# Kernel optimization log

Hardware: AMD Instinct MI355X
Metric: run time of the kernel (lower is better)

The kernel has to match this reference:

```python
import jax, jax.numpy as jnp
import numpy as np

H_IMG = 128; W_IMG = 128
TANFOVX = 0.5; TANFOVY = 0.5
SCALE_MOD = 1.0
C0 = 0.28209479177387814
C1 = 0.4886025119029199
C2 = (1.0925484305920792, -1.0925484305920792, 0.31539156525252005, -1.0925484305920792, 0.5462742152960396)
C3 = (-0.5900435899266435, 2.890611442640554, -0.4570457994644658, 0.3731763325901154, -0.4570457994644658, 1.445305721320277, -0.5900435899266435)


def quat_to_rot(q):
    q = q / jnp.linalg.norm(q, axis=-1, keepdims=True)
    r, x, y, z = q[..., 0], q[..., 1], q[..., 2], q[..., 3]
    row0 = jnp.stack([1 - 2 * (y * y + z * z), 2 * (x * y - r * z), 2 * (x * z + r * y)], -1)
    row1 = jnp.stack([2 * (x * y + r * z), 1 - 2 * (x * x + z * z), 2 * (y * z - r * x)], -1)
    row2 = jnp.stack([2 * (x * z - r * y), 2 * (y * z + r * x), 1 - 2 * (x * x + y * y)], -1)
    return jnp.stack([row0, row1, row2], -2)  # [P,3,3]


def eval_sh(sh, d):
    # sh: [P,16,3], d: [P,3] unit view directions -> RGB per gaussian (degree 3)
    x, y, z = d[:, 0:1], d[:, 1:2], d[:, 2:3]
    res = C0 * sh[:, 0]
    res = res - C1 * y * sh[:, 1] + C1 * z * sh[:, 2] - C1 * x * sh[:, 3]
    xx, yy, zz = x * x, y * y, z * z
    xy, yz, xz = x * y, y * z, x * z
    res = (res + C2[0] * xy * sh[:, 4] + C2[1] * yz * sh[:, 5]
           + C2[2] * (2 * zz - xx - yy) * sh[:, 6] + C2[3] * xz * sh[:, 7]
           + C2[4] * (xx - yy) * sh[:, 8])
    res = (res + C3[0] * y * (3 * xx - yy) * sh[:, 9] + C3[1] * xy * z * sh[:, 10]
           + C3[2] * y * (4 * zz - xx - yy) * sh[:, 11]
           + C3[3] * z * (2 * zz - 3 * xx - 3 * yy) * sh[:, 12]
           + C3[4] * x * (4 * zz - xx - yy) * sh[:, 13]
           + C3[5] * z * (xx - yy) * sh[:, 14] + C3[6] * x * (xx - 3 * yy) * sh[:, 15])
    return jnp.maximum(res + 0.5, 0.0)


def _render_one(means, sh, opac, scales, rots, bg, target, view, proj, campos):
    P = means.shape[0]
    fx = W_IMG / (2.0 * TANFOVX)
    fy = H_IMG / (2.0 * TANFOVY)
    ones = jnp.ones((P, 1), means.dtype)
    xyz1 = jnp.concatenate([means, ones], axis=1)
    hom = xyz1 @ proj.T                                   # [P,4]
    p_w = 1.0 / (hom[:, 3] + 1e-7)
    p_proj = hom[:, :3] * p_w[:, None]
    p_view = xyz1 @ view.T
    depth = p_view[:, 2]
    in_front = depth > 0.2

    # 3D covariance: Sigma = R diag(s) (R diag(s))^T
    R = quat_to_rot(rots)
    M = R * (scales * SCALE_MOD)[:, None, :]
    Sigma = M @ jnp.swapaxes(M, 1, 2)                     # [P,3,3]

    # EWA Jacobian -> 2D covariance
    tz = depth
    txc = jnp.clip(p_view[:, 0] / tz, -1.3 * TANFOVX, 1.3 * TANFOVX) * tz
    tyc = jnp.clip(p_view[:, 1] / tz, -1.3 * TANFOVY, 1.3 * TANFOVY) * tz
    zp = jnp.zeros_like(tz)
    J = jnp.stack([jnp.stack([fx / tz, zp, -fx * txc / (tz * tz)], -1),
                   jnp.stack([zp, fy / tz, -fy * tyc / (tz * tz)], -1)], -2)  # [P,2,3]
    T = J @ view[:3, :3]
    cov2d = T @ Sigma @ jnp.swapaxes(T, 1, 2)             # [P,2,2]
    c00 = cov2d[:, 0, 0] + 0.3
    c11 = cov2d[:, 1, 1] + 0.3
    c01 = cov2d[:, 0, 1]
    det = c00 * c11 - c01 * c01
    valid = in_front & (det > 1e-12)
    inv_det = 1.0 / jnp.where(det > 1e-12, det, 1.0)
    conic = jnp.stack([c11 * inv_det, -c01 * inv_det, c00 * inv_det], -1)
    mid = 0.5 * (c00 + c11)
    lam = mid + jnp.sqrt(jnp.maximum(mid * mid - det, 0.1))
    radii = jnp.where(valid, jnp.ceil(3.0 * jnp.sqrt(lam)), 0.0)

    # NDC -> pixel centers
    px = ((p_proj[:, 0] + 1.0) * W_IMG - 1.0) * 0.5
    py = ((p_proj[:, 1] + 1.0) * H_IMG - 1.0) * 0.5

    dirs = means - campos[None]
    dirs = dirs / jnp.linalg.norm(dirs, axis=-1, keepdims=True)
    colors = eval_sh(sh, dirs)                            # [P,3]

    # front-to-back depth order (same per-pixel order as the tile sort)
    order = jnp.argsort(depth)
    inv_order = jnp.argsort(order)
    px_s, py_s = px[order], py[order]
    con_s = conic[order]
    col_s = colors[order]
    op_s = opac[order, 0]
    val_s = valid[order]

    xs = jnp.arange(W_IMG, dtype=means.dtype)
    ys = jnp.arange(H_IMG, dtype=means.dtype)
    dx = px_s[:, None, None] - xs[None, None, :]          # [P,1,W] -> [P,H,W]
    dy = py_s[:, None, None] - ys[None, :, None]
    power = (-0.5 * (con_s[:, 0, None, None] * dx * dx + con_s[:, 2, None, None] * dy * dy)
             - con_s[:, 1, None, None] * dx * dy)         # [P,H,W]
    alpha = jnp.minimum(0.99, op_s[:, None, None] * jnp.exp(jnp.minimum(power, 0.0)))
    keep = (power <= 0.0) & (alpha >= 1.0 / 255.0) & val_s[:, None, None]
    alpha = jnp.where(keep, alpha, 0.0)
    trans = jnp.cumprod(1.0 - alpha, axis=0)
    T_exc = jnp.concatenate([jnp.ones((1, H_IMG, W_IMG), alpha.dtype), trans[:-1]], axis=0)
    w = alpha * T_exc                                     # per-gaussian pixel weights
    T_final = trans[-1]
    color = jnp.einsum('phw,pc->chw', w, col_s) + T_final[None] * bg[:, None, None]
    alpha_img = (1.0 - T_final)[None]
    est_color = jnp.einsum('phw,chw->pc', w, target)[inv_order]
    est_weight = w.sum(axis=(1, 2))[inv_order, None]
    return color, alpha_img, est_color, est_weight, radii


def reference(means3D, sh, opacities, scales, rotations, target_image, bg, viewmatrix, projmatrix, campos):
    f = jax.vmap(_render_one, in_axes=(0, 0, 0, 0, 0, 0, 0, None, None, None))
    return f(means3D, sh, opacities, scales, rotations, bg, target_image, viewmatrix, projmatrix, campos)


def setup_inputs() -> dict:
    key = jax.random.key(0)
    ks = jax.random.split(key, 8)
    B, P, K = 2, 1024, 16
    xy = jax.random.normal(ks[0], (B, P, 2), jnp.float32) * 1.5
    z = jax.random.uniform(ks[1], (B, P, 1), jnp.float32, 2.0, 6.0)
    means3D = jnp.concatenate([xy, z], -1)
    sh = jax.random.normal(ks[2], (B, P, K, 3), jnp.float32) * 0.3
    opacities = jax.random.uniform(ks[3], (B, P, 1), jnp.float32)
    scales = jax.random.uniform(ks[4], (B, P, 3), jnp.float32, 0.01, 0.08)
    rotations = jax.random.normal(ks[5], (B, P, 4), jnp.float32)
    target_image = jax.random.uniform(ks[6], (B, 3, H_IMG, W_IMG), jnp.float32)
    bg = jax.random.uniform(ks[7], (B, 3), jnp.float32)
    view = np.eye(4, dtype=np.float32)  # camera at origin, +z forward
    znear, zfar = 0.01, 100.0
    proj = np.zeros((4, 4), np.float32)
    proj[0, 0] = 1.0 / TANFOVX
    proj[1, 1] = 1.0 / TANFOVY
    proj[2, 2] = zfar / (zfar - znear)
    proj[2, 3] = -(zfar * znear) / (zfar - znear)
    proj[3, 2] = 1.0
    return {"means3D": means3D, "sh": sh, "opacities": opacities, "scales": scales,
            "rotations": rotations, "target_image": target_image, "bg": bg,
            "viewmatrix": jnp.asarray(view), "projmatrix": jnp.asarray(proj @ view),
            "campos": jnp.zeros((3,), jnp.float32)}
```

## Files before the change

### kernel.cpp

```cpp
#include <hip/hip_runtime.h>
#include <math.h>

#define HI 128
#define WI 128
#define BB 2
#define PG 1024
#define NE (BB*PG)
#define NTILES 128
#define NRED 16
#define MAGIC_HI 0xFEEDFACECAFE0000ULL
#define MASK_HI  0xFFFFFFFFFFFF0000ULL

#define OFF_ALPHA (BB*3*HI*WI)
#define OFF_ESTC  (OFF_ALPHA + BB*HI*WI)
#define OFF_ESTW  (OFF_ESTC + BB*PG*3)
#define OFF_RADII (OFF_ESTW + BB*PG)

struct PC {
  float px, py, ex, ey;
  float A, B, C, op;
  unsigned key;
  float radii;
};

__device__ __forceinline__ PC proj_cull(int e,
    const float* __restrict__ means, const float* __restrict__ opac,
    const float* __restrict__ scales, const float* __restrict__ rots,
    const float* __restrict__ vm, const float* __restrict__ pm)
{
  PC o;
  float mx = means[e*3+0], my = means[e*3+1], mz = means[e*3+2];

  float hom0 = pm[0]*mx + pm[1]*my + pm[2]*mz + pm[3];
  float hom1 = pm[4]*mx + pm[5]*my + pm[6]*mz + pm[7];
  float hom3 = pm[12]*mx + pm[13]*my + pm[14]*mz + pm[15];
  float p_w  = 1.0f / (hom3 + 1e-7f);
  float pp0 = hom0 * p_w, pp1 = hom1 * p_w;

  float pv0   = vm[0]*mx + vm[1]*my + vm[2]*mz  + vm[3];
  float pv1   = vm[4]*mx + vm[5]*my + vm[6]*mz  + vm[7];
  float depth = vm[8]*mx + vm[9]*my + vm[10]*mz + vm[11];

  float qr = rots[e*4+0], qx = rots[e*4+1], qy = rots[e*4+2], qz = rots[e*4+3];
  float qn = sqrtf(qr*qr + qx*qx + qy*qy + qz*qz);
  qr /= qn; qx /= qn; qy /= qn; qz /= qn;
  float R00 = 1.0f-2.0f*(qy*qy+qz*qz), R01 = 2.0f*(qx*qy-qr*qz), R02 = 2.0f*(qx*qz+qr*qy);
  float R10 = 2.0f*(qx*qy+qr*qz), R11 = 1.0f-2.0f*(qx*qx+qz*qz), R12 = 2.0f*(qy*qz-qr*qx);
  float R20 = 2.0f*(qx*qz-qr*qy), R21 = 2.0f*(qy*qz+qr*qx), R22 = 1.0f-2.0f*(qx*qx+qy*qy);

  float s0 = scales[e*3+0], s1 = scales[e*3+1], s2 = scales[e*3+2];
  float M00=R00*s0, M01=R01*s1, M02=R02*s2;
  float M10=R10*s0, M11=R11*s1, M12=R12*s2;
  float M20=R20*s0, M21=R21*s1, M22=R22*s2;
  float S00 = M00*M00+M01*M01+M02*M02;
  float S01 = M00*M10+M01*M11+M02*M12;
  float S02 = M00*M20+M01*M21+M02*M22;
  float S11 = M10*M10+M11*M11+M12*M12;
  float S12 = M10*M20+M11*M21+M12*M22;
  float S22 = M20*M20+M21*M21+M22*M22;

  const float fx = 128.0f, fyc = 128.0f;
  float tz = depth;
  float txc = fminf(fmaxf(pv0/tz, -0.65f), 0.65f) * tz;
  float tyc = fminf(fmaxf(pv1/tz, -0.65f), 0.65f) * tz;
  float J00 = fx/tz,  J02 = -fx*txc/(tz*tz);
  float J11 = fyc/tz, J12 = -fyc*tyc/(tz*tz);

  float T00 = J00*vm[0] + J02*vm[8];
  float T01 = J00*vm[1] + J02*vm[9];
  float T02 = J00*vm[2] + J02*vm[10];
  float T10 = J11*vm[4] + J12*vm[8];
  float T11 = J11*vm[5] + J12*vm[9];
  float T12 = J11*vm[6] + J12*vm[10];

  float TS00 = T00*S00 + T01*S01 + T02*S02;
  float TS01 = T00*S01 + T01*S11 + T02*S12;
  float TS02 = T00*S02 + T01*S12 + T02*S22;
  float TS10 = T10*S00 + T11*S01 + T12*S02;
  float TS11 = T10*S01 + T11*S11 + T12*S12;
  float TS12 = T10*S02 + T11*S12 + T12*S22;

  float c00 = TS00*T00 + TS01*T01 + TS02*T02 + 0.3f;
  float c01 = TS00*T10 + TS01*T11 + TS02*T12;
  float c11 = TS10*T10 + TS11*T11 + TS12*T12 + 0.3f;

  float det = c00*c11 - c01*c01;
  bool valid = (depth > 0.2f) && (det > 1e-12f);
  float inv_det = 1.0f / (det > 1e-12f ? det : 1.0f);
  o.A =  c11 * inv_det;
  o.B = -c01 * inv_det;
  o.C =  c00 * inv_det;
  float mid = 0.5f * (c00 + c11);
  float lam = mid + sqrtf(fmaxf(mid*mid - det, 0.1f));
  o.radii = valid ? ceilf(3.0f * sqrtf(lam)) : 0.0f;

  o.px = ((pp0 + 1.0f)*WI - 1.0f)*0.5f;
  o.py = ((pp1 + 1.0f)*HI - 1.0f)*0.5f;

  float opv = opac[e];
  o.op = opv;
  float tau = logf(255.0f * opv);
  bool rok = valid && (tau > 0.0f);
  o.ex = rok ? sqrtf(2.0f*tau*c00) + 0.02f : -1e9f;
  o.ey = rok ? sqrtf(2.0f*tau*c11) + 0.02f : -1e9f;

  unsigned u = __float_as_uint(depth);
  o.key = (u >> 31) ? ~u : (u | 0x80000000u);
  return o;
}

__device__ __forceinline__ void sh_color(int e,
    const float* __restrict__ sh, const float* __restrict__ means,
    const float* __restrict__ campos, float col[3])
{
  float mx = means[e*3+0], my = means[e*3+1], mz = means[e*3+2];
  float dxr = mx - campos[0], dyr = my - campos[1], dzr = mz - campos[2];
  float dn = sqrtf(dxr*dxr + dyr*dyr + dzr*dzr);
  float x = dxr/dn, y = dyr/dn, z = dzr/dn;
  float xx=x*x, yy=y*y, zz=z*z, xy=x*y, yz=y*z, xz=x*z;
  const float* S = sh + e*48;
  #pragma unroll
  for (int c = 0; c < 3; ++c) {
    float r = 0.28209479177387814f * S[0+c];
    r -= 0.4886025119029199f * y * S[3+c];
    r += 0.4886025119029199f * z * S[6+c];
    r -= 0.4886025119029199f * x * S[9+c];
    r += 1.0925484305920792f  * xy * S[12+c];
    r += -1.0925484305920792f * yz * S[15+c];
    r += 0.31539156525252005f * (2.0f*zz-xx-yy) * S[18+c];
    r += -1.0925484305920792f * xz * S[21+c];
    r += 0.5462742152960396f  * (xx-yy) * S[24+c];
    r += -0.5900435899266435f * y * (3.0f*xx-yy) * S[27+c];
    r += 2.890611442640554f   * xy * z * S[30+c];
    r += -0.4570457994644658f * y * (4.0f*zz-xx-yy) * S[33+c];
    r += 0.3731763325901154f  * z * (2.0f*zz-3.0f*xx-3.0f*yy) * S[36+c];
    r += -0.4570457994644658f * x * (4.0f*zz-xx-yy) * S[39+c];
    r += 1.445305721320277f   * z * (xx-yy) * S[42+c];
    r += -0.5900435899266435f * x * (xx-3.0f*yy) * S[45+c];
    col[c] = fmaxf(r + 0.5f, 0.0f);
  }
}

__global__ __launch_bounds__(256) void fused_kernel(
    const float* __restrict__ means, const float* __restrict__ sh,
    const float* __restrict__ opac, const float* __restrict__ scales,
    const float* __restrict__ rots, const float* __restrict__ vm,
    const float* __restrict__ pm, const float* __restrict__ campos,
    const float* __restrict__ target, const float* __restrict__ bg,
    float4* __restrict__ pval, unsigned long long* __restrict__ flags,
    int* __restrict__ pgid, float* __restrict__ out)
{
  const int t = threadIdx.x;
  const int blk = blockIdx.x;

  __shared__ unsigned long long skey[PG];
  __shared__ float4 recA[256], recB[256], colC[256], stgt[256];
  __shared__ float  wmat[32][264];
  __shared__ int    scount;
  __shared__ int    scnt[64], soff[65];

  if (blk < NTILES) {
    const int b = blk >> 6, tile = blk & 63;
    const int tx0i = (tile & 7) * 16, ty0i = (tile >> 3) * 16;
    const int xi = tx0i + (t & 15), yi = ty0i + (t >> 4);
    const float fxp = (float)xi, fyp = (float)yi;
    const float rx0 = (float)tx0i, ry0 = (float)ty0i;

    if (t == 0) scount = 0;
    stgt[t] = make_float4(target[((b*3+0)*HI + yi)*WI + xi],
                          target[((b*3+1)*HI + yi)*WI + xi],
                          target[((b*3+2)*HI + yi)*WI + xi], 1.0f);
    __syncthreads();

    for (int k = 0; k < 4; ++k) {
      int ci = k*256 + t;
      PC r = proj_cull((b<<10)+ci, means, opac, scales, rots, vm, pm);
      bool ok = (r.px + r.ex >= rx0) && (r.px - r.ex <= rx0 + 15.0f)
             && (r.py + r.ey >= ry0) && (r.py - r.ey <= ry0 + 15.0f);
      if (ok) {
        int pos = atomicAdd(&scount, 1);
        skey[pos] = (((unsigned long long)r.key) << 10) | (unsigned)ci;
      }
    }
    __syncthreads();
    int total = scount;

    if (total > 1) {
      if (total <= 64) {
        if (t < 64) {
          unsigned long long v = (t < total) ? skey[t] : ~0ull;
          #pragma unroll
          for (int k = 2; k <= 64; k <<= 1) {
            bool dirAsc = ((t & k) == 0);
            #pragma unroll
            for (int j = k >> 1; j > 0; j >>= 1) {
              unsigned long long o = __shfl_xor(v, j, 64);
              bool takeMin = (((t & j) == 0) == dirAsc);
              bool less = v < o;
              v = (takeMin == less) ? v : o;
            }
          }
          if (t < total) skey[t] = v;
        }
        __syncthreads();
      } else {
        int M = 64; while (M < total) M <<= 1;
        for (int i = total + t; i < M; i += 256) skey[i] = ~0ull;
        __syncthreads();
        for (int k = 2; k <= M; k <<= 1)
          for (int j = k >> 1; j > 0; j >>= 1) {
            for (int base = t; base < M; base += 256) {
              int ixj = base ^ j;
              if (ixj > base) {
                unsigned long long a = skey[base], q = skey[ixj];
                bool up = ((base & k) == 0);
                if ((a > q) == up) { skey[base] = q; skey[ixj] = a; }
              }
            }
            __syncthreads();
          }
      }
    }

    float T = 1.0f, a0 = 0.f, a1 = 0.f, a2 = 0.f;

    for (int p0 = 0; p0 < total; p0 += 256) {
      int lim = min(256, total - p0);
      if (p0 + t < total) {
        int gi = (int)(skey[p0 + t] & 1023u);
        int e = (b<<10) + gi;
        PC r = proj_cull(e, means, opac, scales, rots, vm, pm);
        float col[3]; sh_color(e, sh, means, campos, col);
        recA[t] = make_float4(r.px, r.py, r.A, r.B);
        recB[t] = make_float4(r.C, r.op, __int_as_float(gi), 0.f);
        colC[t] = make_float4(col[0], col[1], col[2], 0.f);
      }
      __syncthreads();

      for (int c0 = 0; c0 < lim; c0 += 32) {
        int cc = min(32, lim - c0);
        for (int i = 0; i < cc; ++i) {
          float4 qa = recA[c0+i], qb = recB[c0+i], qc = colC[c0+i];
          float dx = qa.x - fxp, dy = qa.y - fyp;
          float power = -0.5f*(qa.z*dx*dx + qb.x*dy*dy) - qa.w*dx*dy;
          float alpha = fminf(0.99f, qb.y * __expf(power));
          bool keep = (power <= 0.0f) && (alpha >= (1.0f/255.0f));
          float w_ = keep ? alpha * T : 0.0f;
          a0 += w_*qc.x; a1 += w_*qc.y; a2 += w_*qc.z;
          T -= w_;
          wmat[i][t] = w_;
        }
        __syncthreads();
        int row = t >> 3, j = t & 7;
        if (row < cc) {
          float e0=0.f, e1=0.f, e2=0.f, ew=0.f;
          #pragma unroll 8
          for (int k = 0; k < 32; ++k) {
            int p = j + 8*k;
            float w_ = wmat[row][p];
            float4 tg = stgt[p];
            e0 += w_*tg.x; e1 += w_*tg.y; e2 += w_*tg.z; ew += w_;
          }
          #pragma unroll
          for (int o = 4; o; o >>= 1) {
            e0 += __shfl_down(e0, o, 8); e1 += __shfl_down(e1, o, 8);
            e2 += __shfl_down(e2, o, 8); ew += __shfl_down(ew, o, 8);
          }
          if (j == 0) {
            int idx = p0 + c0 + row;
            pgid[blk*PG + idx] = __float_as_int(recB[c0+row].z);
            pval[blk*PG + idx] = make_float4(e0, e1, e2, ew);
          }
        }
        __syncthreads();
      }
    }

    out[((b*3+0)*HI + yi)*WI + xi] = a0 + T * bg[b*3+0];
    out[((b*3+1)*HI + yi)*WI + xi] = a1 + T * bg[b*3+1];
    out[((b*3+2)*HI + yi)*WI + xi] = a2 + T * bg[b*3+2];
    out[OFF_ALPHA + (b*HI + yi)*WI + xi] = 1.0f - T;

    __syncthreads();
    if (t == 0) {
      __threadfence();
      atomicExch(&flags[blk], MAGIC_HI | (unsigned long long)total);
    }
    return;
  }

  const int r = blk - NTILES;
  const int batch = r >> 3, seg = r & 7;

  if (t < 128) {
    int e_own = (batch<<10) + seg*128 + t;
    PC g = proj_cull(e_own, means, opac, scales, rots, vm, pm);
    out[OFF_RADII + e_own] = g.radii;
  }

  float* acc = &wmat[0][0];
  for (int i = t; i < 128*4; i += 256) acc[i] = 0.f;

  if (t < 64) {
    unsigned long long v;
    do { v = atomicAdd(&flags[batch*64 + t], 0ull); }
    while ((v & MASK_HI) != MAGIC_HI);
    scnt[t] = (int)(v & 0xFFFFull);
  }
  __syncthreads();
  __threadfence();

  if (t == 0) {
    int s = 0;
    for (int i = 0; i < 64; ++i) { soff[i] = s; s += scnt[i]; }
    soff[64] = s;
  }
  __syncthreads();
  int E = soff[64];

  for (int idx = t; idx < E; idx += 256) {
    int lo = 0, hi = 63;
    while (lo < hi) { int mid = (lo+hi+1) >> 1; if (soff[mid] <= idx) lo = mid; else hi = mid-1; }
    int tb = batch*64 + lo;
    int j = idx - soff[lo];
    int gi = pgid[tb*PG + j];
    if ((gi >> 7) == seg) {
      float4 v = pval[tb*PG + j];
      int s = gi & 127;
      atomicAdd(&acc[s*4+0], v.x);
      atomicAdd(&acc[s*4+1], v.y);
      atomicAdd(&acc[s*4+2], v.z);
      atomicAdd(&acc[s*4+3], v.w);
    }
  }
  __syncthreads();

  if (t < 128) {
    int e_own = (batch<<10) + seg*128 + t;
    out[OFF_ESTC + e_own*3 + 0] = acc[t*4+0];
    out[OFF_ESTC + e_own*3 + 1] = acc[t*4+1];
    out[OFF_ESTC + e_own*3 + 2] = acc[t*4+2];
    out[OFF_ESTW + e_own]       = acc[t*4+3];
  }
}

extern "C" void kernel_launch(void* const* d_in, const int* in_sizes, int n_in,
                              void* d_out, int out_size, void* d_ws, size_t ws_size,
                              hipStream_t stream) {
  const float* means  = (const float*)d_in[0];
  const float* sh     = (const float*)d_in[1];
  const float* opac   = (const float*)d_in[2];
  const float* scales = (const float*)d_in[3];
  const float* rots   = (const float*)d_in[4];
  const float* target = (const float*)d_in[5];
  const float* bg     = (const float*)d_in[6];
  const float* vm     = (const float*)d_in[7];
  const float* pm     = (const float*)d_in[8];
  const float* campos = (const float*)d_in[9];
  float* out = (float*)d_out;

  float4* pval = (float4*)d_ws;
  unsigned long long* flags = (unsigned long long*)(pval + NTILES*PG);
  int* pgid = (int*)(flags + NTILES);

  fused_kernel<<<NTILES + NRED, 256, 0, stream>>>(
      means, sh, opac, scales, rots, vm, pm, campos, target, bg,
      pval, flags, pgid, out);
}
```

Baseline: 21.57 us.

## Compute per-Gaussian projection and SH once in producer blocks, share via workspace

Sixteen producer blocks now project, cull and evaluate SH colour for each Gaussian once, writing the results to global workspace, then signal with flags. Tile blocks wait on those flags, then read the precomputed records instead of recomputing proj_cull for all 1024 Gaussians plus SH per tile. The producer blocks later also do the per-Gaussian reduction, spinning with s_sleep on tile flags. This removes heavy redundant per-tile math but adds a cross-block dependency and spin-wait latency, and it relies on producer blocks being scheduled first. Flags are never reset, so the scheme is only safe if the workspace is cleared between launches.

Result: slower. 27.86 us (+29.2%).

```diff
diff --git a/kernel.cpp b/kernel.cpp
--- a/kernel.cpp
+++ b/kernel.cpp
@@ -6,10 +6,11 @@
 #define BB 2
 #define PG 1024
 #define NE (BB*PG)
+#define NPROD 16
 #define NTILES 128
-#define NRED 16
-#define MAGIC_HI 0xFEEDFACECAFE0000ULL
-#define MASK_HI  0xFFFFFFFFFFFF0000ULL
+#define MAGIC     0xFEEDFACECAFEBEEFULL
+#define MAGIC_HI  0xFEEDFACECAFE0000ULL
+#define MASK_HI   0xFFFFFFFFFFFF0000ULL
 
 #define OFF_ALPHA (BB*3*HI*WI)
 #define OFF_ESTC  (OFF_ALPHA + BB*HI*WI)
@@ -147,8 +148,13 @@
     const float* __restrict__ rots, const float* __restrict__ vm,
     const float* __restrict__ pm, const float* __restrict__ campos,
     const float* __restrict__ target, const float* __restrict__ bg,
-    float4* __restrict__ pval, unsigned long long* __restrict__ flags,
-    int* __restrict__ pgid, float* __restrict__ out)
+    float4* __restrict__ culk, unsigned int* __restrict__ keyar,
+    float4* __restrict__ recAg, float4* __restrict__ recBg,
+    float4* __restrict__ colCg,
+    float4* __restrict__ pval, int* __restrict__ pgid,
+    unsigned long long* __restrict__ prodflags,
+    unsigned long long* __restrict__ tileflags,
+    float* __restrict__ out)
 {
   const int t = threadIdx.x;
   const int blk = blockIdx.x;
@@ -159,188 +165,202 @@
   __shared__ int    scount;
   __shared__ int    scnt[64], soff[65];
 
-  if (blk < NTILES) {
-    const int b = blk >> 6, tile = blk & 63;
-    const int tx0i = (tile & 7) * 16, ty0i = (tile >> 3) * 16;
-    const int xi = tx0i + (t & 15), yi = ty0i + (t >> 4);
-    const float fxp = (float)xi, fyp = (float)yi;
-    const float rx0 = (float)tx0i, ry0 = (float)ty0i;
-
-    if (t == 0) scount = 0;
-    stgt[t] = make_float4(target[((b*3+0)*HI + yi)*WI + xi],
-                          target[((b*3+1)*HI + yi)*WI + xi],
-                          target[((b*3+2)*HI + yi)*WI + xi], 1.0f);
-    __syncthreads();
-
-    for (int k = 0; k < 4; ++k) {
-      int ci = k*256 + t;
-      PC r = proj_cull((b<<10)+ci, means, opac, scales, rots, vm, pm);
-      bool ok = (r.px + r.ex >= rx0) && (r.px - r.ex <= rx0 + 15.0f)
-             && (r.py + r.ey >= ry0) && (r.py - r.ey <= ry0 + 15.0f);
-      if (ok) {
-        int pos = atomicAdd(&scount, 1);
-        skey[pos] = (((unsigned long long)r.key) << 10) | (unsigned)ci;
+  if (blk < NPROD) {
+    const int batch = blk >> 3, seg = blk & 7;
+    const int e_own = (batch << 10) + seg*128 + (t & 127);
+
+    if (t < 128) {
+      PC g = proj_cull(e_own, means, opac, scales, rots, vm, pm);
+      float col[3]; sh_color(e_own, sh, means, campos, col);
+      culk[e_own]  = make_float4(g.px, g.py, g.ex, g.ey);
+      keyar[e_own] = g.key;
+      recAg[e_own] = make_float4(g.px, g.py, g.A, g.B);
+      recBg[e_own] = make_float4(g.C, g.op, 0.f, 0.f);
+      colCg[e_own] = make_float4(col[0], col[1], col[2], 0.f);
+      out[OFF_RADII + e_own] = g.radii;
+    }
+    __syncthreads();
+    if (t == 0) {
+      __threadfence();
+      atomicExch(&prodflags[blk], MAGIC);
+    }
+
+    float* acc = &wmat[0][0];
+    for (int i = t; i < 128*4; i += 256) acc[i] = 0.f;
+
+    if (t < 64) {
+      unsigned long long v;
+      do { v = atomicAdd(&tileflags[batch*64 + t], 0ull);
+           if ((v & MASK_HI) != MAGIC_HI) __builtin_amdgcn_s_sleep(1);
+      } while ((v & MASK_HI) != MAGIC_HI);
+      scnt[t] = (int)(v & 0xFFFFull);
+    }
+    __syncthreads();
+    __threadfence();
+
+    if (t == 0) {
+      int s = 0;
+      for (int i = 0; i < 64; ++i) { soff[i] = s; s += scnt[i]; }
+      soff[64] = s;
+    }
+    __syncthreads();
+    int E = soff[64];
+
+    for (int idx = t; idx < E; idx += 256) {
+      int lo = 0, hi = 63;
+      while (lo < hi) { int mid = (lo+hi+1) >> 1; if (soff[mid] <= idx) lo = mid; else hi = mid-1; }
+      int tb = batch*64 + lo;
+      int j = idx - soff[lo];
+      int gi = pgid[tb*PG + j];
+      if ((gi >> 7) == seg) {
+        float4 v = pval[tb*PG + j];
+        int s = gi & 127;
+        atomicAdd(&acc[s*4+0], v.x);
+        atomicAdd(&acc[s*4+1], v.y);
+        atomicAdd(&acc[s*4+2], v.z);
+        atomicAdd(&acc[s*4+3], v.w);
       }
     }
     __syncthreads();
-    int total = scount;
-
-    if (total > 1) {
-      if (total <= 64) {
-        if (t < 64) {
-          unsigned long long v = (t < total) ? skey[t] : ~0ull;
+
+    if (t < 128) {
+      out[OFF_ESTC + e_own*3 + 0] = acc[(t&127)*4+0];
+      out[OFF_ESTC + e_own*3 + 1] = acc[(t&127)*4+1];
+      out[OFF_ESTC + e_own*3 + 2] = acc[(t&127)*4+2];
+      out[OFF_ESTW + e_own]       = acc[(t&127)*4+3];
+    }
+    return;
+  }
+
+  const int tblk = blk - NPROD;
+  const int b = tblk >> 6, tile = tblk & 63;
+  const int tx0i = (tile & 7) * 16, ty0i = (tile >> 3) * 16;
+  const int xi = tx0i + (t & 15), yi = ty0i + (t >> 4);
+  const float fxp = (float)xi, fyp = (float)yi;
+  const float rx0 = (float)tx0i, ry0 = (float)ty0i;
+
+  if (t == 0) scount = 0;
+  stgt[t] = make_float4(target[((b*3+0)*HI + yi)*WI + xi],
+                        target[((b*3+1)*HI + yi)*WI + xi],
+                        target[((b*3+2)*HI + yi)*WI + xi], 1.0f);
+
+  if (t < 8) {
+    while (atomicAdd(&prodflags[b*8 + t], 0ull) != MAGIC) __builtin_amdgcn_s_sleep(1);
+  }
+  __syncthreads();
+  __threadfence();
+
+  for (int k = 0; k < 4; ++k) {
+    int ci = k*256 + t;
+    float4 cv = culk[(b<<10) + ci];
+    bool ok = (cv.x + cv.z >= rx0) && (cv.x - cv.z <= rx0 + 15.0f)
+           && (cv.y + cv.w >= ry0) && (cv.y - cv.w <= ry0 + 15.0f);
+    if (ok) {
+      int pos = atomicAdd(&scount, 1);
+      skey[pos] = (((unsigned long long)keyar[(b<<10) + ci]) << 10) | (unsigned)ci;
+    }
+  }
+  __syncthreads();
+  int total = scount;
+
+  if (total > 1) {
+    if (total <= 64) {
+      if (t < 64) {
+        unsigned long long v = (t < total) ? skey[t] : ~0ull;
+        #pragma unroll
+        for (int k = 2; k <= 64; k <<= 1) {
+          bool dirAsc = ((t & k) == 0);
           #pragma unroll
-          for (int k = 2; k <= 64; k <<= 1) {
-            bool dirAsc = ((t & k) == 0);
-            #pragma unroll
-            for (int j = k >> 1; j > 0; j >>= 1) {
-              unsigned long long o = __shfl_xor(v, j, 64);
-              bool takeMin = (((t & j) == 0) == dirAsc);
-              bool less = v < o;
-              v = (takeMin == less) ? v : o;
+          for (int j = k >> 1; j > 0; j >>= 1) {
+            unsigned long long o = __shfl_xor(v, j, 64);
+            bool takeMin = (((t & j) == 0) == dirAsc);
+            bool less = v < o;
+            v = (takeMin == less) ? v : o;
+          }
+        }
+        if (t < total) skey[t] = v;
+      }
+      __syncthreads();
+    } else {
+      int M = 64; while (M < total) M <<= 1;
+      for (int i = total + t; i < M; i += 256) skey[i] = ~0ull;
+      __syncthreads();
+      for (int k = 2; k <= M; k <<= 1)
+        for (int j = k >> 1; j > 0; j >>= 1) {
+          for (int base = t; base < M; base += 256) {
+            int ixj = base ^ j;
+            if (ixj > base) {
+              unsigned long long a = skey[base], q = skey[ixj];
+              bool up = ((base & k) == 0);
+              if ((a > q) == up) { skey[base] = q; skey[ixj] = a; }
             }
           }
-          if (t < total) skey[t] = v;
-        }
-        __syncthreads();
-      } else {
-        int M = 64; while (M < total) M <<= 1;
-        for (int i = total + t; i < M; i += 256) skey[i] = ~0ull;
-        __syncthreads();
-        for (int k = 2; k <= M; k <<= 1)
-          for (int j = k >> 1; j > 0; j >>= 1) {
-            for (int base = t; base < M; base += 256) {
-              int ixj = base ^ j;
-              if (ixj > base) {
-                unsigned long long a = skey[base], q = skey[ixj];
-                bool up = ((base & k) == 0);
-                if ((a > q) == up) { skey[base] = q; skey[ixj] = a; }
-              }
-            }
-            __syncthreads();
-          }
-      }
-    }
-
-    float T = 1.0f, a0 = 0.f, a1 = 0.f, a2 = 0.f;
-
-    for (int p0 = 0; p0 < total; p0 += 256) {
-      int lim = min(256, total - p0);
-      if (p0 + t < total) {
-        int gi = (int)(skey[p0 + t] & 1023u);
-        int e = (b<<10) + gi;
-        PC r = proj_cull(e, means, opac, scales, rots, vm, pm);
-        float col[3]; sh_color(e, sh, means, campos, col);
-        recA[t] = make_float4(r.px, r.py, r.A, r.B);
-        recB[t] = make_float4(r.C, r.op, __int_as_float(gi), 0.f);
-        colC[t] = make_float4(col[0], col[1], col[2], 0.f);
+          __syncthreads();
+        }
+    }
+  }
+
+  float T = 1.0f, a0 = 0.f, a1 = 0.f, a2 = 0.f;
+
+  for (int p0 = 0; p0 < total; p0 += 256) {
+    int lim = min(256, total - p0);
+    if (p0 + t < total) {
+      int gi = (int)(skey[p0 + t] & 1023u);
+      int e = (b<<10) + gi;
+      float4 rb = recBg[e];
+      rb.z = __int_as_float(gi);
+      recA[t] = recAg[e]; recB[t] = rb; colC[t] = colCg[e];
+    }
+    __syncthreads();
+
+    for (int c0 = 0; c0 < lim; c0 += 32) {
+      int cc = min(32, lim - c0);
+      for (int i = 0; i < cc; ++i) {
+        float4 qa = recA[c0+i], qb = recB[c0+i], qc = colC[c0+i];
+        float dx = qa.x - fxp, dy = qa.y - fyp;
+        float power = -0.5f*(qa.z*dx*dx + qb.x*dy*dy) - qa.w*dx*dy;
+        float alpha = fminf(0.99f, qb.y * __expf(power));
+        bool keep = (power <= 0.0f) && (alpha >= (1.0f/255.0f));
+        float w_ = keep ? alpha * T : 0.0f;
+        a0 += w_*qc.x; a1 += w_*qc.y; a2 += w_*qc.z;
+        T -= w_;
+        wmat[i][t] = w_;
       }
       __syncthreads();
-
-      for (int c0 = 0; c0 < lim; c0 += 32) {
-        int cc = min(32, lim - c0);
-        for (int i = 0; i < cc; ++i) {
-          float4 qa = recA[c0+i], qb = recB[c0+i], qc = colC[c0+i];
-          float dx = qa.x - fxp, dy = qa.y - fyp;
-          float power = -0.5f*(qa.z*dx*dx + qb.x*dy*dy) - qa.w*dx*dy;
-          float alpha = fminf(0.99f, qb.y * __expf(power));
-          bool keep = (power <= 0.0f) && (alpha >= (1.0f/255.0f));
-          float w_ = keep ? alpha * T : 0.0f;
-          a0 += w_*qc.x; a1 += w_*qc.y; a2 += w_*qc.z;
-          T -= w_;
-          wmat[i][t] = w_;
-        }
-        __syncthreads();
-        int row = t >> 3, j = t & 7;
-        if (row < cc) {
-          float e0=0.f, e1=0.f, e2=0.f, ew=0.f;
-          #pragma unroll 8
-          for (int k = 0; k < 32; ++k) {
-            int p = j + 8*k;
-            float w_ = wmat[row][p];
-            float4 tg = stgt[p];
-            e0 += w_*tg.x; e1 += w_*tg.y; e2 += w_*tg.z; ew += w_;
-          }
-          #pragma unroll
-          for (int o = 4; o; o >>= 1) {
-            e0 += __shfl_down(e0, o, 8); e1 += __shfl_down(e1, o, 8);
-            e2 += __shfl_down(e2, o, 8); ew += __shfl_down(ew, o, 8);
-          }
-          if (j == 0) {
-            int idx = p0 + c0 + row;
-            pgid[blk*PG + idx] = __float_as_int(recB[c0+row].z);
-            pval[blk*PG + idx] = make_float4(e0, e1, e2, ew);
-          }
-        }
-        __syncthreads();
+      int row = t >> 3, j = t & 7;
+      if (row < cc) {
+        float e0=0.f, e1=0.f, e2=0.f, ew=0.f;
+        #pragma unroll 8
+        for (int k = 0; k < 32; ++k) {
+          int p = j + 8*k;
+          float w_ = wmat[row][p];
+          float4 tg = stgt[p];
+          e0 += w_*tg.x; e1 += w_*tg.y; e2 += w_*tg.z; ew += w_;
+        }
+        #pragma unroll
+        for (int o = 4; o; o >>= 1) {
+          e0 += __shfl_down(e0, o, 8); e1 += __shfl_down(e1, o, 8);
+          e2 += __shfl_down(e2, o, 8); ew += __shfl_down(ew, o, 8);
+        }
+        if (j == 0) {
+          int idx = p0 + c0 + row;
+          pgid[tblk*PG + idx] = __float_as_int(recB[c0+row].z);
+          pval[tblk*PG + idx] = make_float4(e0, e1, e2, ew);
+        }
       }
-    }
-
-    out[((b*3+0)*HI + yi)*WI + xi] = a0 + T * bg[b*3+0];
-    out[((b*3+1)*HI + yi)*WI + xi] = a1 + T * bg[b*3+1];
-    out[((b*3+2)*HI + yi)*WI + xi] = a2 + T * bg[b*3+2];
-    out[OFF_ALPHA + (b*HI + yi)*WI + xi] = 1.0f - T;
-
-    __syncthreads();
-    if (t == 0) {
-      __threadfence();
-      atomicExch(&flags[blk], MAGIC_HI | (unsigned long long)total);
-    }
-    return;
-  }
-
-  const int r = blk - NTILES;
-  const int batch = r >> 3, seg = r & 7;
-
-  if (t < 128) {
-    int e_own = (batch<<10) + seg*128 + t;
-    PC g = proj_cull(e_own, means, opac, scales, rots, vm, pm);
-    out[OFF_RADII + e_own] = g.radii;
-  }
-
-  float* acc = &wmat[0][0];
-  for (int i = t; i < 128*4; i += 256) acc[i] = 0.f;
-
-  if (t < 64) {
-    unsigned long long v;
-    do { v = atomicAdd(&flags[batch*64 + t], 0ull); }
-    while ((v & MASK_HI) != MAGIC_HI);
-    scnt[t] = (int)(v & 0xFFFFull);
-  }
+      __syncthreads();
+    }
+  }
+
+  out[((b*3+0)*HI + yi)*WI + xi] = a0 + T * bg[b*3+0];
+  out[((b*3+1)*HI + yi)*WI + xi] = a1 + T * bg[b*3+1];
+  out[((b*3+2)*HI + yi)*WI + xi] = a2 + T * bg[b*3+2];
+  out[OFF_ALPHA + (b*HI + yi)*WI + xi] = 1.0f - T;
+
   __syncthreads();
-  __threadfence();
-
   if (t == 0) {
-    int s = 0;
-    for (int i = 0; i < 64; ++i) { soff[i] = s; s += scnt[i]; }
-    soff[64] = s;
-  }
-  __syncthreads();
-  int E = soff[64];
-
-  for (int idx = t; idx < E; idx += 256) {
-    int lo = 0, hi = 63;
-    while (lo < hi) { int mid = (lo+hi+1) >> 1; if (soff[mid] <= idx) lo = mid; else hi = mid-1; }
-    int tb = batch*64 + lo;
-    int j = idx - soff[lo];
-    int gi = pgid[tb*PG + j];
-    if ((gi >> 7) == seg) {
-      float4 v = pval[tb*PG + j];
-      int s = gi & 127;
-      atomicAdd(&acc[s*4+0], v.x);
-      atomicAdd(&acc[s*4+1], v.y);
-      atomicAdd(&acc[s*4+2], v.z);
-      atomicAdd(&acc[s*4+3], v.w);
-    }
-  }
-  __syncthreads();
-
-  if (t < 128) {
-    int e_own = (batch<<10) + seg*128 + t;
-    out[OFF_ESTC + e_own*3 + 0] = acc[t*4+0];
-    out[OFF_ESTC + e_own*3 + 1] = acc[t*4+1];
-    out[OFF_ESTC + e_own*3 + 2] = acc[t*4+2];
-    out[OFF_ESTW + e_own]       = acc[t*4+3];
+    __threadfence();
+    atomicExch(&tileflags[tblk], MAGIC_HI | (unsigned long long)total);
   }
 }
 
@@ -359,11 +379,18 @@
   const float* campos = (const float*)d_in[9];
   float* out = (float*)d_out;
 
-  float4* pval = (float4*)d_ws;
-  unsigned long long* flags = (unsigned long long*)(pval + NTILES*PG);
-  int* pgid = (int*)(flags + NTILES);
-
-  fused_kernel<<<NTILES + NRED, 256, 0, stream>>>(
+  float4* culk  = (float4*)d_ws;
+  float4* recAg = culk + NE;
+  float4* recBg = recAg + NE;
+  float4* colCg = recBg + NE;
+  float4* pval  = colCg + NE;
+  unsigned int* keyar = (unsigned int*)(pval + NTILES*PG);
+  int* pgid = (int*)(keyar + NE);
+  unsigned long long* prodflags = (unsigned long long*)(pgid + NTILES*PG);
+  unsigned long long* tileflags = prodflags + NPROD;
+
+  fused_kernel<<<NPROD + NTILES, 256, 0, stream>>>(
       means, sh, opac, scales, rots, vm, pm, campos, target, bg,
-      pval, flags, pgid, out);
+      culk, keyar, recAg, recBg, colCg, pval, pgid,
+      prodflags, tileflags, out);
 }
```

## Split tiles to 8x16 and overlap blending with per-gaussian reduction via warp specialization

Applied to the files above, without the earlier changes.

Tiles shrink from 16x16 to 8x16 pixels, which doubles the tile blocks to 256 and improves occupancy across the CUs. Inside each block, threads 0-127 blend pixels into a double-buffered weight matrix while threads 128-255 reduce the previous chunk's weights against the target. This overlaps the two phases that previously ran serially between barriers. The reducer blocks now poll 128 tile flags per batch with s_sleep backoff. The cost is more redundant per-tile projection and culling work, and the tail chunk reduction becomes a separate step.

After: 26.99 us. 1.25x slower.

```diff
diff --git a/kernel.cpp b/kernel.cpp
--- a/kernel.cpp
+++ b/kernel.cpp
@@ -6,10 +6,11 @@
 #define BB 2
 #define PG 1024
 #define NE (BB*PG)
-#define NTILES 128
+#define TPB 128
+#define NT2 (BB*TPB)
 #define NRED 16
-#define MAGIC_HI 0xFEEDFACECAFE0000ULL
-#define MASK_HI  0xFFFFFFFFFFFF0000ULL
+#define MAGIC_HI  0xFEEDFACECAFE0000ULL
+#define MASK_HI   0xFFFFFFFFFFFF0000ULL
 
 #define OFF_ALPHA (BB*3*HI*WI)
 #define OFF_ESTC  (OFF_ALPHA + BB*HI*WI)
@@ -147,35 +148,39 @@
     const float* __restrict__ rots, const float* __restrict__ vm,
     const float* __restrict__ pm, const float* __restrict__ campos,
     const float* __restrict__ target, const float* __restrict__ bg,
-    float4* __restrict__ pval, unsigned long long* __restrict__ flags,
-    int* __restrict__ pgid, float* __restrict__ out)
+    float4* __restrict__ pval, int* __restrict__ pgid,
+    unsigned long long* __restrict__ tileflags,
+    float* __restrict__ out)
 {
   const int t = threadIdx.x;
   const int blk = blockIdx.x;
 
   __shared__ unsigned long long skey[PG];
-  __shared__ float4 recA[256], recB[256], colC[256], stgt[256];
-  __shared__ float  wmat[32][264];
+  __shared__ float4 recA[256], recB[256], colC[256];
+  __shared__ float4 stgt[128];
+  __shared__ float  wmat[2][32][132];
   __shared__ int    scount;
-  __shared__ int    scnt[64], soff[65];
-
-  if (blk < NTILES) {
-    const int b = blk >> 6, tile = blk & 63;
-    const int tx0i = (tile & 7) * 16, ty0i = (tile >> 3) * 16;
-    const int xi = tx0i + (t & 15), yi = ty0i + (t >> 4);
+  __shared__ int    scnt[128], soff[129];
+
+  if (blk < NT2) {
+    const int b = blk >> 7, tile = blk & 127;
+    const int tx0i = (tile & 15) * 8, ty0i = (tile >> 4) * 16;
+    const int xi = tx0i + (t & 7), yi = ty0i + (t >> 3);
+    const float rx0 = (float)tx0i, ry0 = (float)ty0i;
     const float fxp = (float)xi, fyp = (float)yi;
-    const float rx0 = (float)tx0i, ry0 = (float)ty0i;
 
     if (t == 0) scount = 0;
-    stgt[t] = make_float4(target[((b*3+0)*HI + yi)*WI + xi],
-                          target[((b*3+1)*HI + yi)*WI + xi],
-                          target[((b*3+2)*HI + yi)*WI + xi], 1.0f);
+    if (t < 128) {
+      stgt[t] = make_float4(target[((b*3+0)*HI + yi)*WI + xi],
+                            target[((b*3+1)*HI + yi)*WI + xi],
+                            target[((b*3+2)*HI + yi)*WI + xi], 1.0f);
+    }
     __syncthreads();
 
     for (int k = 0; k < 4; ++k) {
       int ci = k*256 + t;
       PC r = proj_cull((b<<10)+ci, means, opac, scales, rots, vm, pm);
-      bool ok = (r.px + r.ex >= rx0) && (r.px - r.ex <= rx0 + 15.0f)
+      bool ok = (r.px + r.ex >= rx0) && (r.px - r.ex <= rx0 + 7.0f)
              && (r.py + r.ey >= ry0) && (r.py - r.ey <= ry0 + 15.0f);
       if (ok) {
         int pos = atomicAdd(&scount, 1);
@@ -237,59 +242,93 @@
       }
       __syncthreads();
 
-      for (int c0 = 0; c0 < lim; c0 += 32) {
+      int nch = (lim + 31) >> 5;
+      for (int ch = 0; ch < nch; ++ch) {
+        int c0 = ch << 5;
         int cc = min(32, lim - c0);
-        for (int i = 0; i < cc; ++i) {
-          float4 qa = recA[c0+i], qb = recB[c0+i], qc = colC[c0+i];
-          float dx = qa.x - fxp, dy = qa.y - fyp;
-          float power = -0.5f*(qa.z*dx*dx + qb.x*dy*dy) - qa.w*dx*dy;
-          float alpha = fminf(0.99f, qb.y * __expf(power));
-          bool keep = (power <= 0.0f) && (alpha >= (1.0f/255.0f));
-          float w_ = keep ? alpha * T : 0.0f;
-          a0 += w_*qc.x; a1 += w_*qc.y; a2 += w_*qc.z;
-          T -= w_;
-          wmat[i][t] = w_;
-        }
-        __syncthreads();
-        int row = t >> 3, j = t & 7;
-        if (row < cc) {
+        int buf = ch & 1;
+        if (t < 128) {
+          for (int i = 0; i < cc; ++i) {
+            float4 qa = recA[c0+i], qb = recB[c0+i], qc = colC[c0+i];
+            float dx = qa.x - fxp, dy = qa.y - fyp;
+            float power = -0.5f*(qa.z*dx*dx + qb.x*dy*dy) - qa.w*dx*dy;
+            float alpha = fminf(0.99f, qb.y * __expf(power));
+            bool keep = (power <= 0.0f) && (alpha >= (1.0f/255.0f));
+            float w_ = keep ? alpha * T : 0.0f;
+            a0 += w_*qc.x; a1 += w_*qc.y; a2 += w_*qc.z;
+            T -= w_;
+            wmat[buf][i][t] = w_;
+          }
+        } else if (ch > 0) {
+          int ts = t - 128;
+          int row = ts >> 2, j = ts & 3;
+          int pc0 = (ch-1) << 5;
           float e0=0.f, e1=0.f, e2=0.f, ew=0.f;
           #pragma unroll 8
           for (int k = 0; k < 32; ++k) {
-            int p = j + 8*k;
-            float w_ = wmat[row][p];
+            int p = j + 4*k;
+            float w_ = wmat[buf^1][row][p];
             float4 tg = stgt[p];
             e0 += w_*tg.x; e1 += w_*tg.y; e2 += w_*tg.z; ew += w_;
           }
-          #pragma unroll
-          for (int o = 4; o; o >>= 1) {
-            e0 += __shfl_down(e0, o, 8); e1 += __shfl_down(e1, o, 8);
-            e2 += __shfl_down(e2, o, 8); ew += __shfl_down(ew, o, 8);
-          }
+          e0 += __shfl_down(e0, 2, 4); e1 += __shfl_down(e1, 2, 4);
+          e2 += __shfl_down(e2, 2, 4); ew += __shfl_down(ew, 2, 4);
+          e0 += __shfl_down(e0, 1, 4); e1 += __shfl_down(e1, 1, 4);
+          e2 += __shfl_down(e2, 1, 4); ew += __shfl_down(ew, 1, 4);
           if (j == 0) {
-            int idx = p0 + c0 + row;
-            pgid[blk*PG + idx] = __float_as_int(recB[c0+row].z);
+            int idx = p0 + pc0 + row;
+            pgid[blk*PG + idx] = __float_as_int(recB[pc0+row].z);
             pval[blk*PG + idx] = make_float4(e0, e1, e2, ew);
           }
         }
         __syncthreads();
       }
-    }
-
-    out[((b*3+0)*HI + yi)*WI + xi] = a0 + T * bg[b*3+0];
-    out[((b*3+1)*HI + yi)*WI + xi] = a1 + T * bg[b*3+1];
-    out[((b*3+2)*HI + yi)*WI + xi] = a2 + T * bg[b*3+2];
-    out[OFF_ALPHA + (b*HI + yi)*WI + xi] = 1.0f - T;
+      {
+        int lc0 = (nch-1) << 5;
+        int lcc = lim - lc0;
+        int lbuf = (nch-1) & 1;
+        if (t < 128) {
+          int row = t >> 2, j = t & 3;
+          if (row < lcc) {
+            float e0=0.f, e1=0.f, e2=0.f, ew=0.f;
+            #pragma unroll 8
+            for (int k = 0; k < 32; ++k) {
+              int p = j + 4*k;
+              float w_ = wmat[lbuf][row][p];
+              float4 tg = stgt[p];
+              e0 += w_*tg.x; e1 += w_*tg.y; e2 += w_*tg.z; ew += w_;
+            }
+            e0 += __shfl_down(e0, 2, 4); e1 += __shfl_down(e1, 2, 4);
+            e2 += __shfl_down(e2, 2, 4); ew += __shfl_down(ew, 2, 4);
+            e0 += __shfl_down(e0, 1, 4); e1 += __shfl_down(e1, 1, 4);
+            e2 += __shfl_down(e2, 1, 4); ew += __shfl_down(ew, 1, 4);
+            if (j == 0) {
+              int idx = p0 + lc0 + row;
+              pgid[blk*PG + idx] = __float_as_int(recB[lc0+row].z);
+              pval[blk*PG + idx] = make_float4(e0, e1, e2, ew);
+            }
+          }
+        }
+        __syncthreads();
+      }
+    }
+
+    if (t < 128) {
+      out[((b*3+0)*HI + yi)*WI + xi] = a0 + T * bg[b*3+0];
+      out[((b*3+1)*HI + yi)*WI + xi] = a1 + T * bg[b*3+1];
+      out[((b*3+2)*HI + yi)*WI + xi] = a2 + T * bg[b*3+2];
+      out[OFF_ALPHA + (b*HI + yi)*WI + xi] = 1.0f - T;
+    }
 
     __syncthreads();
     if (t == 0) {
       __threadfence();
-      atomicExch(&flags[blk], MAGIC_HI | (unsigned long long)total);
+      atomicExch(&tileflags[blk], MAGIC_HI | (unsigned long long)total);
     }
     return;
   }
 
-  const int r = blk - NTILES;
+  const int r = blk - NT2;
   const int batch = r >> 3, seg = r & 7;
 
   if (t < 128) {
@@ -298,13 +337,14 @@
     out[OFF_RADII + e_own] = g.radii;
   }
 
-  float* acc = &wmat[0][0];
+  float* acc = &wmat[0][0][0];
   for (int i = t; i < 128*4; i += 256) acc[i] = 0.f;
 
-  if (t < 64) {
+  if (t < 128) {
     unsigned long long v;
-    do { v = atomicAdd(&flags[batch*64 + t], 0ull); }
-    while ((v & MASK_HI) != MAGIC_HI);
+    do { v = atomicAdd(&tileflags[batch*TPB + t], 0ull);
+         if ((v & MASK_HI) != MAGIC_HI) __builtin_amdgcn_s_sleep(1);
+    } while ((v & MASK_HI) != MAGIC_HI);
     scnt[t] = (int)(v & 0xFFFFull);
   }
   __syncthreads();
@@ -312,16 +352,16 @@
 
   if (t == 0) {
     int s = 0;
-    for (int i = 0; i < 64; ++i) { soff[i] = s; s += scnt[i]; }
-    soff[64] = s;
+    for (int i = 0; i < TPB; ++i) { soff[i] = s; s += scnt[i]; }
+    soff[TPB] = s;
   }
   __syncthreads();
-  int E = soff[64];
+  int E = soff[TPB];
 
   for (int idx = t; idx < E; idx += 256) {
-    int lo = 0, hi = 63;
+    int lo = 0, hi = TPB-1;
     while (lo < hi) { int mid = (lo+hi+1) >> 1; if (soff[mid] <= idx) lo = mid; else hi = mid-1; }
-    int tb = batch*64 + lo;
+    int tb = batch*TPB + lo;
     int j = idx - soff[lo];
     int gi = pgid[tb*PG + j];
     if ((gi >> 7) == seg) {
@@ -360,10 +400,10 @@
   float* out = (float*)d_out;
 
   float4* pval = (float4*)d_ws;
-  unsigned long long* flags = (unsigned long long*)(pval + NTILES*PG);
-  int* pgid = (int*)(flags + NTILES);
-
-  fused_kernel<<<NTILES + NRED, 256, 0, stream>>>(
+  int* pgid = (int*)(pval + NT2*PG);
+  unsigned long long* tileflags = (unsigned long long*)(pgid + NT2*PG);
+
+  fused_kernel<<<NT2 + NRED, 256, 0, stream>>>(
       means, sh, opac, scales, rots, vm, pm, campos, target, bg,
-      pval, flags, pgid, out);
+      pval, pgid, tileflags, out);
 }
```
